# Kernel tuning notes

Measured on AMD Instinct MI355X. Metric: run time of the kernel, lower is better.

The kernel has to match this reference:

```python
import jax, jax.numpy as jnp
import numpy as np
import math

NUM_HEADS = 16
MAX_BIAS = 8.0

def _alibi_slopes(n_heads):
    def slopes(n):
        start = 2.0 ** (-2 ** (-(math.log2(n) - 3)))
        return [start * start ** i for i in range(n)]
    if math.log2(n_heads).is_integer():
        s = slopes(n_heads)
    else:
        p = 2 ** math.floor(math.log2(n_heads))
        s = slopes(p) + slopes(2 * p)[0::2][: n_heads - p]
    return jnp.asarray(np.array(s, dtype=np.float32))

def setup_inputs() -> dict:
    key = jax.random.key(0)
    ks = jax.random.split(key, 5)
    B, S, C = 2, 2048, 1024
    return {
        "x": jax.random.normal(ks[0], (B, S, C), jnp.float32),
        "in_proj_weight": jax.random.normal(ks[1], (3 * C, C), jnp.float32) * (C ** -0.5),
        "in_proj_bias": jax.random.normal(ks[2], (3 * C,), jnp.float32) * 0.02,
        "out_proj_weight": jax.random.normal(ks[3], (C, C), jnp.float32) * (C ** -0.5),
        "out_proj_bias": jax.random.normal(ks[4], (C,), jnp.float32) * 0.02,
    }

def reference(x, in_proj_weight, in_proj_bias, out_proj_weight, out_proj_bias):
    B, S, C = x.shape
    H = NUM_HEADS
    D = C // H
    # fused qkv projection: [B,S,3C] -> [3,B,H,S,D]
    qkv = x @ in_proj_weight.T + in_proj_bias
    qkv = qkv.reshape(B, S, 3, H, D).transpose(2, 0, 3, 1, 4)
    q, k, v = qkv[0], qkv[1], qkv[2]
    # ALiBi bias: slopes[h] * (i - j), clamped above at MAX_BIAS -> [H,S,S]
    slopes = _alibi_slopes(H)
    pos = jnp.arange(S, dtype=jnp.float32)
    rel = pos[:, None] - pos[None, :]  # [S,S]
    bias = jnp.minimum(rel[None, :, :] * slopes[:, None, None], MAX_BIAS)
    # scores [B,H,S,S]
    scores = jnp.einsum("bhqd,bhkd->bhqk", q, k) * (D ** -0.5) + bias[None]
    probs = jax.nn.softmax(scores, axis=-1)
    out = jnp.einsum("bhqk,bhkd->bhqd", probs, v)
    out = out.transpose(0, 2, 1, 3).reshape(B, S, C)
    return out @ out_proj_weight.T + out_proj_bias
```

## Files before the change

### kernel.cpp

```cpp
#include <hip/hip_runtime.h>
#include <hip/hip_bf16.h>

typedef __bf16 bf16;
typedef __bf16 bf16x8 __attribute__((ext_vector_type(8)));
typedef __bf16 bf16x4 __attribute__((ext_vector_type(4)));
typedef float  f32x4  __attribute__((ext_vector_type(4)));
typedef short  s16x4  __attribute__((ext_vector_type(4)));

#define LOG2E 1.44269504088896340736f


__device__ __forceinline__ void gl_lds16(const void* g, void* l) {
  __builtin_amdgcn_global_load_lds((__attribute__((address_space(1))) void*)g,
                                   (__attribute__((address_space(3))) void*)l,
                                   16, 0, 0);
}

#if __has_builtin(__builtin_amdgcn_mfma_f32_16x16x16bf16_1k)
__device__ __forceinline__ f32x4 mfma16(s16x4 a, s16x4 b, f32x4 c) {
  return __builtin_amdgcn_mfma_f32_16x16x16bf16_1k(a, b, c, 0, 0, 0);
}
#else
__device__ __forceinline__ f32x4 mfma16(s16x4 a, s16x4 b, f32x4 c) {
  f32x4 d;
  asm volatile("v_mfma_f32_16x16x16_bf16 %0, %1, %2, %3\n\ts_nop 7\n\ts_nop 3"
               : "=v"(d) : "v"(a), "v"(b), "v"(c));
  return d;
}
#endif

__device__ __forceinline__ s16x4 as_s16x4(bf16x4 v) {
  union { bf16x4 h; s16x4 s; } u; u.h = v; return u.s;
}

__global__ void cvt3_kernel(const float* __restrict__ x,
                            const float* __restrict__ w1,
                            const float* __restrict__ w2,
                            bf16* __restrict__ xb,
                            bf16* __restrict__ w1b,
                            bf16* __restrict__ w2b) {
  const int NX = 1048576, NW1 = 786432, NW2 = 262144;
  const int total = NX + NW1 + NW2;
  int i = blockIdx.x * blockDim.x + threadIdx.x;
  const int stride = gridDim.x * blockDim.x;
  for (; i < total; i += stride) {
    const float* s; bf16* d; int j;
    if (i < NX)            { s = x;  d = xb;  j = i; }
    else if (i < NX + NW1) { s = w1; d = w1b; j = i - NX; }
    else                   { s = w2; d = w2b; j = i - NX - NW1; }
    f32x4 v = ((const f32x4*)s)[j];
    bf16x4 o;
    o[0] = (bf16)v[0]; o[1] = (bf16)v[1]; o[2] = (bf16)v[2]; o[3] = (bf16)v[3];
    ((bf16x4*)d)[j] = o;
  }
}

template<int EPI>
__global__ __launch_bounds__(256) void gemm_bt(const bf16* __restrict__ A,
                                               const bf16* __restrict__ Bw,
                                               const float* __restrict__ bias,
                                               void* __restrict__ outp,
                                               int M, int N, int K) {
  __shared__ bf16 As[128 * 64];
  __shared__ bf16 Bs[128 * 64];
  const int tid  = threadIdx.x;
  const int lane = tid & 63;
  const int w    = tid >> 6;
  const int wm   = w >> 1, wn = w & 1;
  const int mBase = blockIdx.y * 128;
  const int nBase = blockIdx.x * 128;
  const int rl = lane & 15;
  const int qg = lane >> 4;
  const int srow = tid >> 3;
  const int schunk = tid & 7;

  f32x4 acc[4][4] = {};

  for (int k0 = 0; k0 < K; k0 += 64) {
    __syncthreads();
#pragma unroll
    for (int rr = 0; rr < 4; ++rr) {
      int r  = rr * 32 + srow;
      int cs = schunk ^ (r & 7);
      gl_lds16(A  + (size_t)(mBase + r) * K + k0 + cs * 8, As + r * 64 + schunk * 8);
      gl_lds16(Bw + (size_t)(nBase + r) * K + k0 + cs * 8, Bs + r * 64 + schunk * 8);
    }
    __syncthreads();
#pragma unroll
    for (int ks = 0; ks < 2; ++ks) {
      bf16x8 af[4], bfr[4];
      const int cl = ks * 4 + qg;
#pragma unroll
      for (int mf = 0; mf < 4; ++mf) {
        int r = wm * 64 + mf * 16 + rl;
        af[mf] = *(const bf16x8*)(As + r * 64 + (cl ^ (r & 7)) * 8);
      }
#pragma unroll
      for (int nf = 0; nf < 4; ++nf) {
        int r = wn * 64 + nf * 16 + rl;
        bfr[nf] = *(const bf16x8*)(Bs + r * 64 + (cl ^ (r & 7)) * 8);
      }
#pragma unroll
      for (int mf = 0; mf < 4; ++mf)
#pragma unroll
        for (int nf = 0; nf < 4; ++nf)
          acc[mf][nf] = __builtin_amdgcn_mfma_f32_16x16x32_bf16(af[mf], bfr[nf],
                                                                acc[mf][nf], 0, 0, 0);
    }
  }

#pragma unroll
  for (int mf = 0; mf < 4; ++mf) {
#pragma unroll
    for (int nf = 0; nf < 4; ++nf) {
      int n = nBase + wn * 64 + nf * 16 + rl;
      float bv = bias[n];
#pragma unroll
      for (int j = 0; j < 4; ++j) {
        int m = mBase + wm * 64 + mf * 16 + qg * 4 + j;
        float val = acc[mf][nf][j] + bv;
        if (EPI == 0) {
          int t = n >> 10, rem = n & 1023;
          int h = rem >> 6, d = rem & 63;
          int b = m >> 11, s = m & 2047;
          bf16* q = (bf16*)outp;
          size_t hb = (size_t)(b * 16 + h);
          if (t == 0) {
            q[(hb * 2048 + s) * 64 + d] = (bf16)(val * (0.125f * LOG2E));
          } else if (t == 1) {
            q[4194304 + (hb * 2048 + s) * 64 + d] = (bf16)val;
          } else {
            q[8388608 + (hb * 64 + d) * 2048 + s] = (bf16)val;
          }
        } else {
          ((float*)outp)[(size_t)m * N + n] = val;
        }
      }
    }
  }
}

__global__ __launch_bounds__(256) void attn_kernel(const bf16* __restrict__ qkv,
                                                   bf16* __restrict__ attout) {
  constexpr int S = 2048;
  __shared__ bf16 Ks[64 * 64];
  __shared__ bf16 Vt[80 * 64];

  const int tid  = threadIdx.x;
  const int lane = tid & 63;
  const int w    = tid >> 6;
  const int id = blockIdx.x;
  const int bh = (id & 7) * 4 + ((id >> 3) & 3);
  const int qt = id >> 5;
  const int h  = bh & 15;
  const size_t headoff = (size_t)bh * 131072;
  const bf16* Qg = qkv + headoff;
  const bf16* Kg = qkv + 4194304 + headoff;
  const bf16* Vg = qkv + 8388608 + headoff;

  const int rl = lane & 15;
  const int qg = lane >> 4;
  const int srow = tid >> 3;
  const int schunk = tid & 7;

  for (int i = tid; i < 16 * 64; i += 256)
    Vt[64 * 64 + i] = (bf16)1.0f;

  const int qrow = qt * 64 + w * 16 + rl;
  bf16x8 qf[2];
  qf[0] = *(const bf16x8*)(Qg + (size_t)qrow * 64 + qg * 8);
  qf[1] = *(const bf16x8*)(Qg + (size_t)qrow * 64 + 32 + qg * 8);

  int koff[4][2];
#pragma unroll
  for (int cf = 0; cf < 4; ++cf) {
    int r = cf * 16 + rl, r7 = r & 7;
#pragma unroll
    for (int ks = 0; ks < 2; ++ks)
      koff[cf][ks] = r * 64 + (((ks * 4 + qg) ^ r7) << 3);
  }
  int voff[4][5];
#pragma unroll
  for (int dg = 0; dg < 5; ++dg) {
    int row = dg * 16 + rl, r7 = row & 7;
#pragma unroll
    for (int cf = 0; cf < 4; ++cf)
      voff[cf][dg] = row * 64 + ((((cf << 1) + (qg >> 1)) ^ r7) << 3) + ((qg & 1) << 2);
  }

  const int cs8 = (schunk ^ (srow & 7)) * 8;
  const bf16* ksrc = Kg + (size_t)srow * 64 + cs8;
  const bf16* vsrc = Vg + (size_t)srow * 2048 + cs8;
  bf16* kdst = Ks + srow * 64 + schunk * 8;
  bf16* vdst = Vt + srow * 64 + schunk * 8;

  const float slope2 = exp2f(-0.5f * (float)(h + 1)) * LOG2E;
  const float nslope = -slope2;
  const float kstep  = slope2 * 64.0f;
  float basep = slope2 * (float)(qrow - qg * 4);
  float Mm    = 8.0f * LOG2E;

  f32x4 o[5] = {};

  for (int kt = 0; kt < S / 64; ++kt) {
    __syncthreads();
    gl_lds16(ksrc,             kdst);
    gl_lds16(ksrc + 32 * 64,   kdst + 32 * 64);
    gl_lds16(vsrc,             vdst);
    gl_lds16(vsrc + 32 * 2048, vdst + 32 * 64);
    ksrc += 64 * 64; vsrc += 64;
    __syncthreads();

    f32x4 sc[4] = {};
#pragma unroll
    for (int cf = 0; cf < 4; ++cf)
#pragma unroll
      for (int ks = 0; ks < 2; ++ks) {
        bf16x8 kf = *(const bf16x8*)(Ks + koff[cf][ks]);
        sc[cf] = __builtin_amdgcn_mfma_f32_16x16x32_bf16(kf, qf[ks], sc[cf], 0, 0, 0);
      }

    float t[4][4];
#pragma unroll
    for (int cf = 0; cf < 4; ++cf)
#pragma unroll
      for (int j = 0; j < 4; ++j)
        t[cf][j] = sc[cf][j] + fminf(__builtin_fmaf(nslope, (float)(cf * 16 + j), basep), Mm);

    float mxa = fmaxf(fmaxf(t[0][0], t[0][1]), fmaxf(t[0][2], t[0][3]));
    float mxb = fmaxf(fmaxf(t[1][0], t[1][1]), fmaxf(t[1][2], t[1][3]));
    float mxc = fmaxf(fmaxf(t[2][0], t[2][1]), fmaxf(t[2][2], t[2][3]));
    float mxd = fmaxf(fmaxf(t[3][0], t[3][1]), fmaxf(t[3][2], t[3][3]));
    float mx = fmaxf(fmaxf(mxa, mxb), fmaxf(mxc, mxd));
    mx = fmaxf(mx, __shfl_xor(mx, 16));
    mx = fmaxf(mx, __shfl_xor(mx, 32));

    bf16x4 pav[4];
    if (__any(mx > 8.0f)) {
      float d = fmaxf(mx, 0.0f);
      basep -= d; Mm -= d;
      float alpha = exp2f(-d);
      float av[4];
#pragma unroll
      for (int j = 0; j < 4; ++j)
        av[j] = __shfl(alpha, qg * 4 + j);
#pragma unroll
      for (int dg = 0; dg < 5; ++dg)
#pragma unroll
        for (int j = 0; j < 4; ++j)
          o[dg][j] *= av[j];
#pragma unroll
      for (int cf = 0; cf < 4; ++cf)
#pragma unroll
        for (int j = 0; j < 4; ++j)
          pav[cf][j] = (bf16)exp2f(t[cf][j] - d);
    } else {
#pragma unroll
      for (int cf = 0; cf < 4; ++cf)
#pragma unroll
        for (int j = 0; j < 4; ++j)
          pav[cf][j] = (bf16)exp2f(t[cf][j]);
    }

#pragma unroll
    for (int cf = 0; cf < 4; ++cf) {
      s16x4 pa = as_s16x4(pav[cf]);
#pragma unroll
      for (int dg = 0; dg < 5; ++dg) {
        s16x4 vb = *(const s16x4*)(Vt + voff[cf][dg]);
        o[dg] = mfma16(pa, vb, o[dg]);
      }
    }

    basep -= kstep;
  }

  float inv[4];
#pragma unroll
  for (int j = 0; j < 4; ++j)
    inv[j] = 1.0f / o[4][j];

  const int b = bh >> 4;
#pragma unroll
  for (int dg = 0; dg < 4; ++dg)
#pragma unroll
    for (int j = 0; j < 4; ++j) {
      int row = qt * 64 + w * 16 + qg * 4 + j;
      int col = h * 64 + dg * 16 + rl;
      attout[((size_t)b * 2048 + row) * 1024 + col] = (bf16)(o[dg][j] * inv[j]);
    }
}

extern "C" void kernel_launch(void* const* d_in, const int* in_sizes, int n_in,
                              void* d_out, int out_size, void* d_ws, size_t ws_size,
                              hipStream_t stream) {
  const float* x  = (const float*)d_in[0];
  const float* w1 = (const float*)d_in[1];
  const float* b1 = (const float*)d_in[2];
  const float* w2 = (const float*)d_in[3];
  const float* b2 = (const float*)d_in[4];
  float* out = (float*)d_out;

  char* ws = (char*)d_ws;
  bf16* xb    = (bf16*)(ws);
  bf16* w1b   = (bf16*)(ws + 8388608);
  bf16* w2b   = (bf16*)(ws + 14680064);
  bf16* qkvb  = (bf16*)(ws + 16777216);
  bf16* attnb = (bf16*)(ws + 41943040);

  cvt3_kernel<<<2048, 256, 0, stream>>>(x, w1, w2, xb, w1b, w2b);
  gemm_bt<0><<<dim3(24, 32), 256, 0, stream>>>(xb, w1b, b1, (void*)qkvb, 4096, 3072, 1024);
  attn_kernel<<<1024, 256, 0, stream>>>(qkvb, attnb);
  gemm_bt<1><<<dim3(8, 32), 256, 0, stream>>>(attnb, w2b, b2, (void*)out, 4096, 1024, 1024);
}
```

Measured before the change: 168.4 us.

## Skip negligible ALiBi key tiles, use 16x16x32 MFMA for PV, rebalance heads

Each query tile now works out, from the ALiBi slope, which key tiles can only hold negligible probability. It stops the key loop early and skips the bias arithmetic on tiles where the clamp always applies. The PV product moves from 16x16x16 MFMA to 16x16x32, with P repacked through cross-lane shuffles and the row-sum ones moved to their own LDS buffer. Block-to-head mapping pairs steep and shallow heads per XCD to balance load, and s_setprio is added around the MFMA sections. Truncating the key range drops contributions below a threshold, which risks small accuracy loss.

```diff
diff --git a/kernel.cpp b/kernel.cpp
--- a/kernel.cpp
+++ b/kernel.cpp
@@ -5,7 +5,6 @@
 typedef __bf16 bf16x8 __attribute__((ext_vector_type(8)));
 typedef __bf16 bf16x4 __attribute__((ext_vector_type(4)));
 typedef float  f32x4  __attribute__((ext_vector_type(4)));
-typedef short  s16x4  __attribute__((ext_vector_type(4)));
 
 #define LOG2E 1.44269504088896340736f
 
@@ -16,21 +15,16 @@
                                    16, 0, 0);
 }
 
-#if __has_builtin(__builtin_amdgcn_mfma_f32_16x16x16bf16_1k)
-__device__ __forceinline__ f32x4 mfma16(s16x4 a, s16x4 b, f32x4 c) {
-  return __builtin_amdgcn_mfma_f32_16x16x16bf16_1k(a, b, c, 0, 0, 0);
-}
-#else
-__device__ __forceinline__ f32x4 mfma16(s16x4 a, s16x4 b, f32x4 c) {
-  f32x4 d;
-  asm volatile("v_mfma_f32_16x16x16_bf16 %0, %1, %2, %3\n\ts_nop 7\n\ts_nop 3"
-               : "=v"(d) : "v"(a), "v"(b), "v"(c));
-  return d;
-}
-#endif
-
-__device__ __forceinline__ s16x4 as_s16x4(bf16x4 v) {
-  union { bf16x4 h; s16x4 s; } u; u.h = v; return u.s;
+__device__ __forceinline__ unsigned cvt_pk(float lo, float hi) {
+  unsigned r;
+  asm("v_cvt_pk_bf16_f32 %0, %1, %2" : "=v"(r) : "v"(lo), "v"(hi));
+  return r;
+}
+
+__device__ __forceinline__ bf16x8 bits8(const unsigned* w) {
+  union { unsigned u[4]; bf16x8 v; } u;
+  u.u[0] = w[0]; u.u[1] = w[1]; u.u[2] = w[2]; u.u[3] = w[3];
+  return u.v;
 }
 
 __global__ void cvt3_kernel(const float* __restrict__ x,
@@ -142,17 +136,20 @@
 
 __global__ __launch_bounds__(256) void attn_kernel(const bf16* __restrict__ qkv,
                                                    bf16* __restrict__ attout) {
-  constexpr int S = 2048;
   __shared__ bf16 Ks[64 * 64];
-  __shared__ bf16 Vt[80 * 64];
+  __shared__ bf16 Vt[64 * 64];
+  __shared__ bf16 ONES[16 * 64];
 
   const int tid  = threadIdx.x;
   const int lane = tid & 63;
   const int w    = tid >> 6;
-  const int id = blockIdx.x;
-  const int bh = (id & 7) * 4 + ((id >> 3) & 3);
-  const int qt = id >> 5;
-  const int h  = bh & 15;
+  const int id  = blockIdx.x;
+  const int xcd = id & 7;
+  const int sel = (id >> 3) & 1;
+  const int b   = (id >> 4) & 1;
+  const int qt  = id >> 5;
+  const int h   = sel ? (15 - xcd) : xcd;
+  const int bh  = b * 16 + h;
   const size_t headoff = (size_t)bh * 131072;
   const bf16* Qg = qkv + headoff;
   const bf16* Kg = qkv + 4194304 + headoff;
@@ -162,16 +159,16 @@
   const int qg = lane >> 4;
   const int srow = tid >> 3;
   const int schunk = tid & 7;
-
-  for (int i = tid; i < 16 * 64; i += 256)
-    Vt[64 * 64 + i] = (bf16)1.0f;
+  const int cs8 = (schunk ^ (srow & 7)) * 8;
+
+  ((bf16x4*)ONES)[tid] = bf16x4{(bf16)1.f, (bf16)1.f, (bf16)1.f, (bf16)1.f};
 
   const int qrow = qt * 64 + w * 16 + rl;
   bf16x8 qf[2];
   qf[0] = *(const bf16x8*)(Qg + (size_t)qrow * 64 + qg * 8);
   qf[1] = *(const bf16x8*)(Qg + (size_t)qrow * 64 + 32 + qg * 8);
 
-  int koff[4][2];
+  int koff[4][2], ooff[2];
 #pragma unroll
   for (int cf = 0; cf < 4; ++cf) {
     int r = cf * 16 + rl, r7 = r & 7;
@@ -179,16 +176,10 @@
     for (int ks = 0; ks < 2; ++ks)
       koff[cf][ks] = r * 64 + (((ks * 4 + qg) ^ r7) << 3);
   }
-  int voff[4][5];
-#pragma unroll
-  for (int dg = 0; dg < 5; ++dg) {
-    int row = dg * 16 + rl, r7 = row & 7;
-#pragma unroll
-    for (int cf = 0; cf < 4; ++cf)
-      voff[cf][dg] = row * 64 + ((((cf << 1) + (qg >> 1)) ^ r7) << 3) + ((qg & 1) << 2);
-  }
-
-  const int cs8 = (schunk ^ (srow & 7)) * 8;
+#pragma unroll
+  for (int ks = 0; ks < 2; ++ks)
+    ooff[ks] = rl * 64 + (((ks * 4 + qg) ^ (rl & 7)) << 3);
+
   const bf16* ksrc = Kg + (size_t)srow * 64 + cs8;
   const bf16* vsrc = Vg + (size_t)srow * 2048 + cs8;
   bf16* kdst = Ks + srow * 64 + schunk * 8;
@@ -200,9 +191,15 @@
   float basep = slope2 * (float)(qrow - qg * 4);
   float Mm    = 8.0f * LOG2E;
 
+  const float q0f = (float)(qt * 64);
+  int ktEnd = (int)floorf((q0f + 63.f + 40.f / slope2) * (1.f / 64.f)) + 1;
+  if (ktEnd > 32) ktEnd = 32;
+  int ktClamp = (int)floorf((q0f - 63.f - 11.6f / slope2) * (1.f / 64.f)) + 1;
+  if (ktClamp < 0) ktClamp = 0;
+
   f32x4 o[5] = {};
 
-  for (int kt = 0; kt < S / 64; ++kt) {
+  for (int kt = 0; kt < ktEnd; ++kt) {
     __syncthreads();
     gl_lds16(ksrc,             kdst);
     gl_lds16(ksrc + 32 * 64,   kdst + 32 * 64);
@@ -212,6 +209,7 @@
     __syncthreads();
 
     f32x4 sc[4] = {};
+    __builtin_amdgcn_s_setprio(1);
 #pragma unroll
     for (int cf = 0; cf < 4; ++cf)
 #pragma unroll
@@ -219,23 +217,31 @@
         bf16x8 kf = *(const bf16x8*)(Ks + koff[cf][ks]);
         sc[cf] = __builtin_amdgcn_mfma_f32_16x16x32_bf16(kf, qf[ks], sc[cf], 0, 0, 0);
       }
-
-    float t[4][4];
-#pragma unroll
-    for (int cf = 0; cf < 4; ++cf)
-#pragma unroll
-      for (int j = 0; j < 4; ++j)
-        t[cf][j] = sc[cf][j] + fminf(__builtin_fmaf(nslope, (float)(cf * 16 + j), basep), Mm);
-
-    float mxa = fmaxf(fmaxf(t[0][0], t[0][1]), fmaxf(t[0][2], t[0][3]));
-    float mxb = fmaxf(fmaxf(t[1][0], t[1][1]), fmaxf(t[1][2], t[1][3]));
-    float mxc = fmaxf(fmaxf(t[2][0], t[2][1]), fmaxf(t[2][2], t[2][3]));
-    float mxd = fmaxf(fmaxf(t[3][0], t[3][1]), fmaxf(t[3][2], t[3][3]));
+    __builtin_amdgcn_s_setprio(0);
+
+    float pe[4][4];
+    if (kt >= ktClamp) {
+#pragma unroll
+      for (int cf = 0; cf < 4; ++cf)
+#pragma unroll
+        for (int j = 0; j < 4; ++j)
+          pe[cf][j] = sc[cf][j] +
+              fminf(__builtin_fmaf(nslope, (float)(cf * 16 + j), basep), Mm);
+    } else {
+#pragma unroll
+      for (int cf = 0; cf < 4; ++cf)
+#pragma unroll
+        for (int j = 0; j < 4; ++j)
+          pe[cf][j] = sc[cf][j] + Mm;
+    }
+    float mxa = fmaxf(fmaxf(pe[0][0], pe[0][1]), fmaxf(pe[0][2], pe[0][3]));
+    float mxb = fmaxf(fmaxf(pe[1][0], pe[1][1]), fmaxf(pe[1][2], pe[1][3]));
+    float mxc = fmaxf(fmaxf(pe[2][0], pe[2][1]), fmaxf(pe[2][2], pe[2][3]));
+    float mxd = fmaxf(fmaxf(pe[3][0], pe[3][1]), fmaxf(pe[3][2], pe[3][3]));
     float mx = fmaxf(fmaxf(mxa, mxb), fmaxf(mxc, mxd));
     mx = fmaxf(mx, __shfl_xor(mx, 16));
     mx = fmaxf(mx, __shfl_xor(mx, 32));
 
-    bf16x4 pav[4];
     if (__any(mx > 8.0f)) {
       float d = fmaxf(mx, 0.0f);
       basep -= d; Mm -= d;
@@ -253,24 +259,64 @@
       for (int cf = 0; cf < 4; ++cf)
 #pragma unroll
         for (int j = 0; j < 4; ++j)
-          pav[cf][j] = (bf16)exp2f(t[cf][j] - d);
+          pe[cf][j] = exp2f(pe[cf][j] - d);
     } else {
 #pragma unroll
       for (int cf = 0; cf < 4; ++cf)
 #pragma unroll
         for (int j = 0; j < 4; ++j)
-          pav[cf][j] = (bf16)exp2f(t[cf][j]);
-    }
-
+          pe[cf][j] = exp2f(pe[cf][j]);
+    }
+
+    unsigned Wd[4][2];
 #pragma unroll
     for (int cf = 0; cf < 4; ++cf) {
-      s16x4 pa = as_s16x4(pav[cf]);
-#pragma unroll
-      for (int dg = 0; dg < 5; ++dg) {
-        s16x4 vb = *(const s16x4*)(Vt + voff[cf][dg]);
-        o[dg] = mfma16(pa, vb, o[dg]);
-      }
-    }
+      Wd[cf][0] = cvt_pk(pe[cf][0], pe[cf][1]);
+      Wd[cf][1] = cvt_pk(pe[cf][2], pe[cf][3]);
+    }
+    const bool hi32  = (lane & 32) != 0;
+    const bool odd16 = (lane & 16) != 0;
+    unsigned Aown[2], Aoth[2], Bown[2], Both[2];
+#pragma unroll
+    for (int u = 0; u < 2; ++u) {
+      Aown[u] = hi32 ? Wd[1][u] : Wd[0][u];
+      Aoth[u] = (unsigned)__shfl_xor((int)(hi32 ? Wd[0][u] : Wd[1][u]), 32);
+      Bown[u] = hi32 ? Wd[3][u] : Wd[2][u];
+      Both[u] = (unsigned)__shfl_xor((int)(hi32 ? Wd[2][u] : Wd[3][u]), 32);
+    }
+    const bool sendOwn = odd16 ^ hi32;
+    unsigned fa[4], fb[4];
+#pragma unroll
+    for (int u = 0; u < 2; ++u) {
+      unsigned rA = (unsigned)__shfl_xor((int)(sendOwn ? Aown[u] : Aoth[u]), 16);
+      unsigned rB = (unsigned)__shfl_xor((int)(sendOwn ? Bown[u] : Both[u]), 16);
+      fa[u]     = odd16 ? rA : (hi32 ? Aoth[u] : Aown[u]);
+      fa[2 + u] = odd16 ? (hi32 ? Aown[u] : Aoth[u]) : rA;
+      fb[u]     = odd16 ? rB : (hi32 ? Both[u] : Bown[u]);
+      fb[2 + u] = odd16 ? (hi32 ? Bown[u] : Both[u]) : rB;
+    }
+    bf16x8 pa0 = bits8(fa), pa1 = bits8(fb);
+
+    __builtin_amdgcn_s_setprio(1);
+#pragma unroll
+    for (int dg = 0; dg < 4; ++dg) {
+      bf16x8 vb = *(const bf16x8*)(Vt + koff[dg][0]);
+      o[dg] = __builtin_amdgcn_mfma_f32_16x16x32_bf16(pa0, vb, o[dg], 0, 0, 0);
+    }
+    {
+      bf16x8 vb = *(const bf16x8*)(ONES + ooff[0]);
+      o[4] = __builtin_amdgcn_mfma_f32_16x16x32_bf16(pa0, vb, o[4], 0, 0, 0);
+    }
+#pragma unroll
+    for (int dg = 0; dg < 4; ++dg) {
+      bf16x8 vb = *(const bf16x8*)(Vt + koff[dg][1]);
+      o[dg] = __builtin_amdgcn_mfma_f32_16x16x32_bf16(pa1, vb, o[dg], 0, 0, 0);
+    }
+    {
+      bf16x8 vb = *(const bf16x8*)(ONES + ooff[1]);
+      o[4] = __builtin_amdgcn_mfma_f32_16x16x32_bf16(pa1, vb, o[4], 0, 0, 0);
+    }
+    __builtin_amdgcn_s_setprio(0);
 
     basep -= kstep;
   }
@@ -280,7 +326,6 @@
   for (int j = 0; j < 4; ++j)
     inv[j] = 1.0f / o[4][j];
 
-  const int b = bh >> 4;
 #pragma unroll
   for (int dg = 0; dg < 4; ++dg)
 #pragma unroll
```

Result: no change. 169.2 us (+0.5%).
